# Kernel tuning notes

Measured on AMD Instinct MI355X. Metric: run time of the kernel, lower is better.

The kernel has to match this reference:

```python
import jax, jax.numpy as jnp
import numpy as np

N_HEAD = 16

def setup_inputs() -> dict:
    key = jax.random.key(0)
    k0, k1, k2, k3 = jax.random.split(key, 4)
    S, E, H, T = 2048, 1024, N_HEAD, 4096
    d = E // H
    return {
        "x": jax.random.normal(k0, (S, E), jnp.float32),
        "past": jax.random.normal(k1, (2, H, T, d), jnp.float32),  # stacked [pk, pv]
        "W1": jax.random.normal(k2, (E, 3 * E), jnp.float32) * 0.02,  # c_attn (Conv1D k=1 == linear)
        "b1": jnp.zeros((3 * E,), jnp.float32),
        "W2": jax.random.normal(k3, (E, E), jnp.float32) * 0.02,  # c_proj
        "b2": jnp.zeros((E,), jnp.float32),
        "past_length": 2048,
    }


def reference(x, past, W1, b1, W2, b2, past_length):
    H = N_HEAD
    S, E = x.shape
    d = E // H

    c = x @ W1 + b1  # [S, 3E]
    q, k, v = jnp.split(c, 3, axis=1)

    def split_heads(t):  # [S, E] -> [H, S, d]
        return jnp.transpose(t.reshape(S, H, d), (1, 0, 2))

    q, k, v = split_heads(q), split_heads(k), split_heads(v)

    pk, pv = past[0], past[1]  # [H, T, d]
    k = jax.lax.dynamic_update_slice_in_dim(pk, k, past_length, axis=1)
    v = jax.lax.dynamic_update_slice_in_dim(pv, v, past_length, axis=1)

    # attention scores [H, S, T]
    w = jnp.einsum('hid,hjd->hij', q, k) / np.sqrt(d)
    ns = k.shape[1]
    i = jnp.arange(S)[:, None]
    j = jnp.arange(ns)[None, :]
    b = (i >= j - past_length).astype(w.dtype)
    w = w * b - jnp.float32(1e10) * (1 - b)
    w = jax.nn.softmax(w, axis=-1)

    a = jnp.einsum('hij,hjd->hid', w, v)  # [H, S, d]
    # faithful to original: start index clamps to 0 since axis len == S
    a = jax.lax.dynamic_slice_in_dim(a, past_length, S, axis=1)
    a = jnp.transpose(a, (1, 0, 2)).reshape(S, E)  # merge heads

    out = a @ W2 + b2
    new_cache = jnp.stack([k, v], axis=0)
    return out, new_cache
```

## Files before the change

kernel.cpp:

```cpp
#include <hip/hip_runtime.h>
#include <hip/hip_bf16.h>
#include <stdint.h>


#define S_LEN 2048
#define E_DIM 1024
#define NHEAD 16
#define HDIM  64
#define T_LEN 4096
#define PASTL 2048

typedef __bf16 bf16x8 __attribute__((ext_vector_type(8)));
typedef __bf16 bf16x4 __attribute__((ext_vector_type(4)));
typedef __bf16 bf16x2 __attribute__((ext_vector_type(2)));
typedef float  f32x4  __attribute__((ext_vector_type(4)));
typedef float  f32x16 __attribute__((ext_vector_type(16)));
typedef unsigned u32x2 __attribute__((ext_vector_type(2)));

static __device__ __forceinline__ f32x4 mfma_bf16(bf16x8 a, bf16x8 b, f32x4 c) {
  return __builtin_amdgcn_mfma_f32_16x16x32_bf16(a, b, c, 0, 0, 0);
}
static __device__ __forceinline__ f32x16 mfma32(bf16x8 a, bf16x8 b, f32x16 c) {
  return __builtin_amdgcn_mfma_f32_32x32x16_bf16(a, b, c, 0, 0, 0);
}

static __device__ __forceinline__ unsigned int f2bf(float f) {
  union { float f; unsigned int u; } v; v.f = f;
  unsigned int u = v.u;
  return (u + 0x7fffu + ((u >> 16) & 1u)) >> 16;
}

static __device__ __forceinline__ float bf2f(unsigned short u) {
  union { unsigned int u; float f; } v; v.u = (unsigned int)u << 16;
  return v.f;
}

static __device__ __forceinline__ unsigned pkbf(float lo, float hi) {
  bf16x2 t = {(__bf16)lo, (__bf16)hi};
  return __builtin_bit_cast(unsigned, t);
}

#define GLOBAL_LOAD_LDS16(gptr, lptr)                                              \
  __builtin_amdgcn_global_load_lds(                                                \
      (const __attribute__((address_space(1))) unsigned int*)(gptr),               \
      (__attribute__((address_space(3))) unsigned int*)(lptr), 16, 0, 0)

__global__ __launch_bounds__(256) void prep_kernel(
    const float* __restrict__ past, const float* __restrict__ x,
    const float* __restrict__ W1, const float* __restrict__ W2,
    float* __restrict__ cache, unsigned short* __restrict__ kb,
    unsigned short* __restrict__ xb, unsigned short* __restrict__ w1t,
    unsigned short* __restrict__ w2t, unsigned short* __restrict__ vtb) {
  __shared__ float tile[64][65];
  const int bid = blockIdx.x;
  const int tid = threadIdx.x;
  const int tx = tid & 63, ty = tid >> 6;

  if (bid < 512) {
    const int h = bid >> 5;
    const int t0 = (bid & 31) * 64;
    const float* in = past + (size_t)(NHEAD + h) * T_LEN * HDIM;
    unsigned short* outp = vtb + (size_t)h * HDIM * T_LEN;
#pragma unroll
    for (int r = 0; r < 64; r += 4)
      tile[r + ty][tx] = in[(size_t)(t0 + r + ty) * HDIM + tx];
    __syncthreads();
#pragma unroll
    for (int r = 0; r < 64; r += 4)
      outp[(size_t)(r + ty) * T_LEN + t0 + tx] = f2bf(tile[tx][r + ty]);
  } else if (bid < 1536) {
    const float* in;
    unsigned short* outp;
    int rows, cols, c0, r0;
    if (bid < 1280) {
      int u = bid - 512;
      in = W1; outp = w1t; rows = 1024; cols = 3072;
      c0 = (u % 48) * 64; r0 = (u / 48) * 64;
    } else {
      int u = bid - 1280;
      in = W2; outp = w2t; rows = 1024; cols = 1024;
      c0 = (u & 15) * 64; r0 = (u >> 4) * 64;
    }
#pragma unroll
    for (int r = 0; r < 64; r += 4)
      tile[r + ty][tx] = in[(size_t)(r0 + r + ty) * cols + c0 + tx];
    __syncthreads();
#pragma unroll
    for (int r = 0; r < 64; r += 4)
      outp[(size_t)(c0 + r + ty) * rows + r0 + tx] = f2bf(tile[tx][r + ty]);
  } else {
    const int n4p = (2 * NHEAD * PASTL * HDIM) / 4;
    const int n4x = (S_LEN * E_DIM) / 4;
    for (int i = (bid - 1536) * 256 + tid; i < n4p + n4x; i += 2048 * 256) {
      if (i < n4p) {
        int e = i * 4;
        int d = e & 63;
        int t = (e >> 6) & (PASTL - 1);
        int hh = (e >> 17) & (NHEAD - 1);
        int kv = e >> 21;
        size_t full = (((size_t)kv * NHEAD + hh) * T_LEN + t) * HDIM + d;
        float4 v = *(const float4*)(past + full);
        *(float4*)(cache + full) = v;
        if (kv == 0) {
          ushort4 u;
          u.x = f2bf(v.x); u.y = f2bf(v.y); u.z = f2bf(v.z); u.w = f2bf(v.w);
          *(ushort4*)(kb + full) = u;
        }
      } else {
        int j = i - n4p;
        float4 v = ((const float4*)x)[j];
        ushort4 u;
        u.x = f2bf(v.x); u.y = f2bf(v.y); u.z = f2bf(v.z); u.w = f2bf(v.w);
        ((ushort4*)xb)[j] = u;
      }
    }
  }
}

template <int MODE>
__global__ __launch_bounds__(256) void gemm_bt_kernel(
    const unsigned short* __restrict__ A, const unsigned short* __restrict__ Bt,
    const float* __restrict__ bias, int K,
    float* __restrict__ out_f32, unsigned short* __restrict__ qb,
    float* __restrict__ cache_k, float* __restrict__ cache_v,
    unsigned short* __restrict__ kb, unsigned short* __restrict__ vtb) {
  __shared__ alignas(16) unsigned short As[2][64 * 64];
  __shared__ alignas(16) unsigned short Bs[2][128 * 64];
  const int NPX = (MODE == 0) ? 3 : 1;
  const int bid = blockIdx.x;
  const int xcd = bid & 7;
  const int loc = bid >> 3;
  const int n_idx = xcd * NPX + loc % NPX;
  const int m_idx = loc / NPX;
  const int m0 = m_idx * 64, n0 = n_idx * 128;

  const int tid = threadIdx.x;
  const int lane = tid & 63;
  const int w = tid >> 6;
  const int wm = w >> 1, wn = w & 1;
  const int lr = lane & 15;
  const int lg = lane >> 4;

  f32x4 acc[2][4];
#pragma unroll
  for (int i = 0; i < 2; ++i)
#pragma unroll
    for (int j = 0; j < 4; ++j) acc[i][j] = f32x4{0.f, 0.f, 0.f, 0.f};

  const int srow = tid >> 3;
  const int sseg = (tid & 7) ^ (srow & 7);
  const unsigned short* ga0 = A + (size_t)(m0 + srow) * K + sseg * 8;
  const unsigned short* gb0 = Bt + (size_t)(n0 + srow) * K + sseg * 8;

  auto stage = [&](int b, int k0) {
    GLOBAL_LOAD_LDS16(ga0 + k0, (char*)As[b] + tid * 16);
    GLOBAL_LOAD_LDS16(ga0 + (size_t)32 * K + k0, (char*)As[b] + 4096 + tid * 16);
#pragma unroll
    for (int j = 0; j < 4; ++j)
      GLOBAL_LOAD_LDS16(gb0 + (size_t)(32 * j) * K + k0,
                        (char*)Bs[b] + j * 4096 + tid * 16);
  };

  const int NKS = K >> 6;
  stage(0, 0);
  int cur = 0;
  for (int i = 0; i < NKS; ++i) {
    asm volatile("s_waitcnt vmcnt(0)" ::: "memory");
    __builtin_amdgcn_s_barrier();
    __builtin_amdgcn_sched_barrier(0);
    if (i + 1 < NKS) stage(cur ^ 1, (i + 1) * 64);

#pragma unroll
    for (int kk = 0; kk < 2; ++kk) {
      bf16x8 af[2], bfr[4];
#pragma unroll
      for (int mi = 0; mi < 2; ++mi) {
        int row = wm * 32 + mi * 16 + lr;
        int slot = (kk * 4 + lg) ^ (row & 7);
        af[mi] = *reinterpret_cast<const bf16x8*>((const char*)As[cur] + row * 128 + slot * 16);
      }
#pragma unroll
      for (int ni = 0; ni < 4; ++ni) {
        int row = wn * 64 + ni * 16 + lr;
        int slot = (kk * 4 + lg) ^ (row & 7);
        bfr[ni] = *reinterpret_cast<const bf16x8*>((const char*)Bs[cur] + row * 128 + slot * 16);
      }
#pragma unroll
      for (int mi = 0; mi < 2; ++mi)
#pragma unroll
        for (int ni = 0; ni < 4; ++ni)
          acc[mi][ni] = mfma_bf16(af[mi], bfr[ni], acc[mi][ni]);
    }
    cur ^= 1;
  }

#pragma unroll
  for (int ni = 0; ni < 4; ++ni) {
    int n = n0 + wn * 64 + ni * 16 + lr;
    float bv = bias[n];
#pragma unroll
    for (int mi = 0; mi < 2; ++mi) {
      int mbase = m0 + wm * 32 + mi * 16 + lg * 4;
      float v4[4];
#pragma unroll
      for (int r = 0; r < 4; ++r) v4[r] = acc[mi][ni][r] + bv;
      if (MODE == 0) {
        if (n < E_DIM) {
#pragma unroll
          for (int r = 0; r < 4; ++r)
            qb[(size_t)(mbase + r) * E_DIM + n] = f2bf(v4[r] * 0.18033688f);
        } else if (n < 2 * E_DIM) {
          int e = n - E_DIM;
          size_t base = ((size_t)(e >> 6) * T_LEN + (PASTL + mbase)) * HDIM + (e & 63);
#pragma unroll
          for (int r = 0; r < 4; ++r) {
            cache_k[base + (size_t)r * HDIM] = v4[r];
            kb[base + (size_t)r * HDIM] = f2bf(v4[r]);
          }
        } else {
          int e = n - 2 * E_DIM;
          int hh = e >> 6, d = e & 63;
          size_t base = ((size_t)hh * T_LEN + (PASTL + mbase)) * HDIM + d;
#pragma unroll
          for (int r = 0; r < 4; ++r) cache_v[base + (size_t)r * HDIM] = v4[r];
          ushort4 u;
          u.x = f2bf(v4[0]); u.y = f2bf(v4[1]);
          u.z = f2bf(v4[2]); u.w = f2bf(v4[3]);
          *(ushort4*)(vtb + ((size_t)hh * HDIM + d) * T_LEN + PASTL + mbase) = u;
        }
      } else {
#pragma unroll
        for (int r = 0; r < 4; ++r)
          out_f32[(size_t)(mbase + r) * E_DIM + n] = v4[r];
      }
    }
  }
}

__global__ __launch_bounds__(256) void attn_kernel(
    const unsigned short* __restrict__ qb, const unsigned short* __restrict__ kb,
    const unsigned short* __restrict__ vt,
    unsigned short* __restrict__ o_part, float* __restrict__ l_part) {
  __shared__ alignas(16) unsigned short Ks[2][64 * 64];
  __shared__ alignas(16) unsigned short Vs[2][64 * 64];
  const int fid = blockIdx.x;
  const int h = (fid & 7) + ((fid >= 448) ? 8 : 0);
  const int g = (fid >> 3) - ((fid >= 448) ? 56 : 0);
  int x, c;
  if (g < 24) { x = g / 3; c = g - 3 * x; }
  else { int g2 = g - 24; x = 8 + (g2 >> 2); c = g2 & 3; }

  const int tid = threadIdx.x;
  const int w = tid >> 6;
  const int lane = tid & 63;
  const int l31 = lane & 31;
  const int hi = lane >> 5;
  const int hi4 = hi * 4;
  const int q0 = x * 128 + w * 32;

  const unsigned short* qrow = qb + (size_t)(q0 + l31) * E_DIM + h * HDIM + hi * 8;
  bf16x8 qf[4];
#pragma unroll
  for (int kk = 0; kk < 4; ++kk)
    qf[kk] = *reinterpret_cast<const bf16x8*>(qrow + kk * 16);

  const unsigned short* kh = kb + (size_t)h * T_LEN * HDIM;
  const unsigned short* vh = vt + (size_t)h * HDIM * T_LEN;

  const int srow = tid >> 3;
  const int sseg = (tid & 7) ^ (srow & 7);
  const unsigned short* ksrc = kh + (size_t)srow * HDIM + sseg * 8;
  const unsigned short* vsrc = vh + (size_t)srow * T_LEN + sseg * 8;

  f32x16 o0, o1, zc;
#pragma unroll
  for (int i = 0; i < 16; ++i) { o0[i] = 0.f; o1[i] = 0.f; zc[i] = 0.f; }
  float lsum = 0.f;

  const int NTfull = 34 + 2 * x;
  const int tb = c * 16;
  const int te = (tb + 16 < NTfull) ? tb + 16 : NTfull;
  const int NT = te - tb;
  const int tbeg = tb * 64;
  const int qpp = q0 + l31 + PASTL;

  auto stageK = [&](int b, int t0) {
    GLOBAL_LOAD_LDS16(ksrc + (size_t)t0 * HDIM, (char*)Ks[b] + tid * 16);
    GLOBAL_LOAD_LDS16(ksrc + (size_t)(t0 + 32) * HDIM, (char*)Ks[b] + 4096 + tid * 16);
  };
  auto stageV = [&](int b, int t0) {
    GLOBAL_LOAD_LDS16(vsrc + t0, (char*)Vs[b] + tid * 16);
    GLOBAL_LOAD_LDS16(vsrc + t0 + (size_t)32 * T_LEN, (char*)Vs[b] + 4096 + tid * 16);
  };

  stageK(0, tbeg);
  stageV(0, tbeg);
  int cur = 0;
  int t0 = tbeg;
  for (int i = 0; i < NT; ++i, t0 += 64) {
    const bool more = (i + 1 < NT);
    asm volatile("s_waitcnt vmcnt(2)" ::: "memory");
    __builtin_amdgcn_s_barrier();
    __builtin_amdgcn_sched_barrier(0);
    if (more) stageK(cur ^ 1, t0 + 64);

    f32x16 s0, s1;
    __builtin_amdgcn_s_setprio(1);
    {
      int sl = hi ^ (l31 & 7);
      bf16x8 k0 = *reinterpret_cast<const bf16x8*>((const char*)Ks[cur] + l31 * 128 + sl * 16);
      bf16x8 k1 = *reinterpret_cast<const bf16x8*>((const char*)Ks[cur] + (32 + l31) * 128 + sl * 16);
      s0 = mfma32(k0, qf[0], zc);
      s1 = mfma32(k1, qf[0], zc);
    }
#pragma unroll
    for (int kk = 1; kk < 4; ++kk) {
      int sl = (kk * 2 + hi) ^ (l31 & 7);
      bf16x8 k0 = *reinterpret_cast<const bf16x8*>((const char*)Ks[cur] + l31 * 128 + sl * 16);
      bf16x8 k1 = *reinterpret_cast<const bf16x8*>((const char*)Ks[cur] + (32 + l31) * 128 + sl * 16);
      s0 = mfma32(k0, qf[kk], s0);
      s1 = mfma32(k1, qf[kk], s1);
    }
    __builtin_amdgcn_s_setprio(0);

    const bool partial = (t0 + 63 > q0 + PASTL);
    unsigned aw[8], bw[8];
    if (!partial) {
#pragma unroll
      for (int i2 = 0; i2 < 8; ++i2) {
        float p0 = __builtin_amdgcn_exp2f(s0[2 * i2]);
        float p1 = __builtin_amdgcn_exp2f(s0[2 * i2 + 1]);
        float p2 = __builtin_amdgcn_exp2f(s1[2 * i2]);
        float p3 = __builtin_amdgcn_exp2f(s1[2 * i2 + 1]);
        lsum += (p0 + p1) + (p2 + p3);
        aw[i2] = pkbf(p0, p1);
        bw[i2] = pkbf(p2, p3);
      }
    } else {
      const int thr = qpp - t0;
#pragma unroll
      for (int i2 = 0; i2 < 8; ++i2) {
        int r0 = 2 * i2;
        int ko = (r0 & 3) + 8 * (r0 >> 2) + hi4;
        float p0 = __builtin_amdgcn_exp2f(s0[r0]);
        float p1 = __builtin_amdgcn_exp2f(s0[r0 + 1]);
        float p2 = __builtin_amdgcn_exp2f(s1[r0]);
        float p3 = __builtin_amdgcn_exp2f(s1[r0 + 1]);
        if (ko > thr) p0 = 0.f;
        if (ko + 1 > thr) p1 = 0.f;
        if (ko + 32 > thr) p2 = 0.f;
        if (ko + 33 > thr) p3 = 0.f;
        lsum += (p0 + p1) + (p2 + p3);
        aw[i2] = pkbf(p0, p1);
        bw[i2] = pkbf(p2, p3);
      }
    }

    union U4 { unsigned u[4]; bf16x8 v; };
    U4 pa0, pa1, pa2, pa3;
    {
      u32x2 r02 = __builtin_amdgcn_permlane32_swap(aw[0], aw[2], false, false);
      u32x2 r13 = __builtin_amdgcn_permlane32_swap(aw[1], aw[3], false, false);
      pa0.u[0] = r02[0]; pa0.u[1] = r13[0]; pa0.u[2] = r02[1]; pa0.u[3] = r13[1];
      u32x2 r46 = __builtin_amdgcn_permlane32_swap(aw[4], aw[6], false, false);
      u32x2 r57 = __builtin_amdgcn_permlane32_swap(aw[5], aw[7], false, false);
      pa1.u[0] = r46[0]; pa1.u[1] = r57[0]; pa1.u[2] = r46[1]; pa1.u[3] = r57[1];
      u32x2 s02 = __builtin_amdgcn_permlane32_swap(bw[0], bw[2], false, false);
      u32x2 s13 = __builtin_amdgcn_permlane32_swap(bw[1], bw[3], false, false);
      pa2.u[0] = s02[0]; pa2.u[1] = s13[0]; pa2.u[2] = s02[1]; pa2.u[3] = s13[1];
      u32x2 s46 = __builtin_amdgcn_permlane32_swap(bw[4], bw[6], false, false);
      u32x2 s57 = __builtin_amdgcn_permlane32_swap(bw[5], bw[7], false, false);
      pa3.u[0] = s46[0]; pa3.u[1] = s57[0]; pa3.u[2] = s46[1]; pa3.u[3] = s57[1];
    }

    if (more) {
      asm volatile("s_waitcnt vmcnt(2)" ::: "memory");
    } else {
      asm volatile("s_waitcnt vmcnt(0)" ::: "memory");
    }
    __builtin_amdgcn_s_barrier();
    __builtin_amdgcn_sched_barrier(0);
    if (more) stageV(cur ^ 1, t0 + 64);

    __builtin_amdgcn_s_setprio(1);
    {
      int sl = hi ^ (l31 & 7);
      bf16x8 v0 = *reinterpret_cast<const bf16x8*>((const char*)Vs[cur] + l31 * 128 + sl * 16);
      bf16x8 v1 = *reinterpret_cast<const bf16x8*>((const char*)Vs[cur] + (32 + l31) * 128 + sl * 16);
      o0 = mfma32(pa0.v, v0, o0);
      o1 = mfma32(pa0.v, v1, o1);
    }
    {
      int sl = (2 + hi) ^ (l31 & 7);
      bf16x8 v0 = *reinterpret_cast<const bf16x8*>((const char*)Vs[cur] + l31 * 128 + sl * 16);
      bf16x8 v1 = *reinterpret_cast<const bf16x8*>((const char*)Vs[cur] + (32 + l31) * 128 + sl * 16);
      o0 = mfma32(pa1.v, v0, o0);
      o1 = mfma32(pa1.v, v1, o1);
    }
    {
      int sl = (4 + hi) ^ (l31 & 7);
      bf16x8 v0 = *reinterpret_cast<const bf16x8*>((const char*)Vs[cur] + l31 * 128 + sl * 16);
      bf16x8 v1 = *reinterpret_cast<const bf16x8*>((const char*)Vs[cur] + (32 + l31) * 128 + sl * 16);
      o0 = mfma32(pa2.v, v0, o0);
      o1 = mfma32(pa2.v, v1, o1);
    }
    {
      int sl = (6 + hi) ^ (l31 & 7);
      bf16x8 v0 = *reinterpret_cast<const bf16x8*>((const char*)Vs[cur] + l31 * 128 + sl * 16);
      bf16x8 v1 = *reinterpret_cast<const bf16x8*>((const char*)Vs[cur] + (32 + l31) * 128 + sl * 16);
      o0 = mfma32(pa3.v, v0, o0);
      o1 = mfma32(pa3.v, v1, o1);
    }
    __builtin_amdgcn_s_setprio(0);
    cur ^= 1;
  }

  lsum += __shfl_xor(lsum, 32);

  unsigned short* op = o_part + ((size_t)(c * NHEAD + h) * S_LEN) * HDIM;
  float* lp = l_part + (size_t)(c * NHEAD + h) * S_LEN;
  if (hi == 0) lp[q0 + l31] = lsum;
#pragma unroll
  for (int r = 0; r < 16; ++r) {
    int qr = (r & 3) + 8 * (r >> 2) + hi4;
    op[(size_t)(q0 + qr) * HDIM + l31] = f2bf(o0[r]);
    op[(size_t)(q0 + qr) * HDIM + 32 + l31] = f2bf(o1[r]);
  }
}

__global__ __launch_bounds__(256) void attn_merge_kernel(
    const unsigned short* __restrict__ o_part, const float* __restrict__ l_part,
    unsigned short* __restrict__ ab) {
  const int flat = blockIdx.x * 256 + threadIdx.x;
  const int d4 = flat & 15;
  const int row = (flat >> 4) & (S_LEN - 1);
  const int h = flat >> 15;
  const int nc = (row < 1024) ? 3 : 4;
  const size_t cstride_o = (size_t)NHEAD * S_LEN * HDIM;
  const size_t base_o = (((size_t)h * S_LEN) + row) * HDIM + d4 * 4;
  float acc[4] = {0.f, 0.f, 0.f, 0.f};
  float l = 0.f;
  for (int cc = 0; cc < nc; ++cc) {
    ushort4 u = *(const ushort4*)(o_part + cc * cstride_o + base_o);
    acc[0] += bf2f(u.x); acc[1] += bf2f(u.y);
    acc[2] += bf2f(u.z); acc[3] += bf2f(u.w);
    l += l_part[(size_t)cc * NHEAD * S_LEN + (size_t)h * S_LEN + row];
  }
  float inv = 1.f / l;
  ushort4 u;
  u.x = f2bf(acc[0] * inv);
  u.y = f2bf(acc[1] * inv);
  u.z = f2bf(acc[2] * inv);
  u.w = f2bf(acc[3] * inv);
  *(ushort4*)(ab + (size_t)row * E_DIM + h * HDIM + d4 * 4) = u;
}


extern "C" void kernel_launch(void* const* d_in, const int* in_sizes, int n_in,
                              void* d_out, int out_size, void* d_ws, size_t ws_size,
                              hipStream_t stream) {
  (void)in_sizes; (void)n_in; (void)out_size; (void)ws_size;
  const float* x    = (const float*)d_in[0];
  const float* past = (const float*)d_in[1];
  const float* W1   = (const float*)d_in[2];
  const float* b1   = (const float*)d_in[3];
  const float* W2   = (const float*)d_in[4];
  const float* b2   = (const float*)d_in[5];

  float* out = (float*)d_out;
  float* cache_k = out + (size_t)S_LEN * E_DIM;
  float* cache_v = cache_k + (size_t)NHEAD * T_LEN * HDIM;

  char* ws = (char*)d_ws;
  unsigned short* w2t = (unsigned short*)(ws);
  unsigned short* qb  = (unsigned short*)(ws + (size_t)(2u  << 20));
  unsigned short* kb  = (unsigned short*)(ws + (size_t)(6u  << 20));
  unsigned short* vtb = (unsigned short*)(ws + (size_t)(14u << 20));
  unsigned short* xb  = (unsigned short*)(ws + (size_t)(22u << 20));
  unsigned short* ab  = (unsigned short*)(ws + (size_t)(22u << 20));
  unsigned short* w1t = (unsigned short*)(ws + (size_t)(26u << 20));
  unsigned short* o_part = (unsigned short*)(ws + (size_t)(26u << 20));
  float* l_part = (float*)(ws + (size_t)(42u << 20));

  prep_kernel<<<3584, 256, 0, stream>>>(past, x, W1, W2, cache_k, kb, xb, w1t,
                                        w2t, vtb);
  gemm_bt_kernel<0><<<768, 256, 0, stream>>>(
      xb, w1t, b1, 1024, nullptr, qb, cache_k, cache_v, kb, vtb);
  attn_kernel<<<dim3(896), 256, 0, stream>>>(qb, kb, vtb, o_part, l_part);
  attn_merge_kernel<<<(NHEAD * S_LEN * 16) / 256, 256, 0, stream>>>(o_part, l_part, ab);
  gemm_bt_kernel<1><<<256, 256, 0, stream>>>(
      ab, w2t, b2, 1024, out, nullptr, nullptr, nullptr, nullptr, nullptr);
}
```

Baseline: 118.9 us.

## Widen attention KV tile from 64 to 128 keys per iteration

Each loop iteration of the attention kernel now stages and processes 128 keys instead of 64, with larger double-buffered K and V shared-memory tiles and a new V swizzle layout for 256-byte rows. The aim is to halve the number of barriers and pipeline steps per chunk and give more MFMA work between synchronisations. The cost is doubled LDS use, which can cut occupancy, and more registers for the eight P fragments held across the loop. Masking is adjusted with a per-half offset.

```diff
diff --git a/kernel.cpp b/kernel.cpp
--- a/kernel.cpp
+++ b/kernel.cpp
@@ -241,8 +241,8 @@
     const unsigned short* __restrict__ qb, const unsigned short* __restrict__ kb,
     const unsigned short* __restrict__ vt,
     unsigned short* __restrict__ o_part, float* __restrict__ l_part) {
-  __shared__ alignas(16) unsigned short Ks[2][64 * 64];
-  __shared__ alignas(16) unsigned short Vs[2][64 * 64];
+  __shared__ alignas(16) unsigned short Ks[2][128 * 64];
+  __shared__ alignas(16) unsigned short Vs[2][64 * 128];
   const int fid = blockIdx.x;
   const int h = (fid & 7) + ((fid >= 448) ? 8 : 0);
   const int g = (fid >> 3) - ((fid >= 448) ? 56 : 0);
@@ -270,146 +270,145 @@
   const int srow = tid >> 3;
   const int sseg = (tid & 7) ^ (srow & 7);
   const unsigned short* ksrc = kh + (size_t)srow * HDIM + sseg * 8;
-  const unsigned short* vsrc = vh + (size_t)srow * T_LEN + sseg * 8;
+  const int vrow = tid >> 4;
+  const int vseg = (tid & 15) ^ (vrow & 7);
+  const unsigned short* vsrc = vh + (size_t)vrow * T_LEN + vseg * 8;
 
   f32x16 o0, o1, zc;
 #pragma unroll
   for (int i = 0; i < 16; ++i) { o0[i] = 0.f; o1[i] = 0.f; zc[i] = 0.f; }
   float lsum = 0.f;
 
-  const int NTfull = 34 + 2 * x;
-  const int tb = c * 16;
-  const int te = (tb + 16 < NTfull) ? tb + 16 : NTfull;
+  const int NT2full = 17 + x;
+  const int tb = c * 8;
+  const int te = (tb + 8 < NT2full) ? tb + 8 : NT2full;
   const int NT = te - tb;
-  const int tbeg = tb * 64;
+  const int tbeg = tb * 128;
   const int qpp = q0 + l31 + PASTL;
 
   auto stageK = [&](int b, int t0) {
-    GLOBAL_LOAD_LDS16(ksrc + (size_t)t0 * HDIM, (char*)Ks[b] + tid * 16);
-    GLOBAL_LOAD_LDS16(ksrc + (size_t)(t0 + 32) * HDIM, (char*)Ks[b] + 4096 + tid * 16);
+#pragma unroll
+    for (int j = 0; j < 4; ++j)
+      GLOBAL_LOAD_LDS16(ksrc + (size_t)(t0 + 32 * j) * HDIM,
+                        (char*)Ks[b] + j * 4096 + tid * 16);
   };
   auto stageV = [&](int b, int t0) {
-    GLOBAL_LOAD_LDS16(vsrc + t0, (char*)Vs[b] + tid * 16);
-    GLOBAL_LOAD_LDS16(vsrc + t0 + (size_t)32 * T_LEN, (char*)Vs[b] + 4096 + tid * 16);
+#pragma unroll
+    for (int j = 0; j < 4; ++j)
+      GLOBAL_LOAD_LDS16(vsrc + (size_t)(16 * j) * T_LEN + t0,
+                        (char*)Vs[b] + j * 4096 + tid * 16);
   };
 
   stageK(0, tbeg);
   stageV(0, tbeg);
   int cur = 0;
   int t0 = tbeg;
-  for (int i = 0; i < NT; ++i, t0 += 64) {
+  for (int i = 0; i < NT; ++i, t0 += 128) {
     const bool more = (i + 1 < NT);
-    asm volatile("s_waitcnt vmcnt(2)" ::: "memory");
+    asm volatile("s_waitcnt vmcnt(4)" ::: "memory");
     __builtin_amdgcn_s_barrier();
     __builtin_amdgcn_sched_barrier(0);
-    if (more) stageK(cur ^ 1, t0 + 64);
-
-    f32x16 s0, s1;
-    __builtin_amdgcn_s_setprio(1);
-    {
-      int sl = hi ^ (l31 & 7);
-      bf16x8 k0 = *reinterpret_cast<const bf16x8*>((const char*)Ks[cur] + l31 * 128 + sl * 16);
-      bf16x8 k1 = *reinterpret_cast<const bf16x8*>((const char*)Ks[cur] + (32 + l31) * 128 + sl * 16);
-      s0 = mfma32(k0, qf[0], zc);
-      s1 = mfma32(k1, qf[0], zc);
-    }
-#pragma unroll
-    for (int kk = 1; kk < 4; ++kk) {
-      int sl = (kk * 2 + hi) ^ (l31 & 7);
-      bf16x8 k0 = *reinterpret_cast<const bf16x8*>((const char*)Ks[cur] + l31 * 128 + sl * 16);
-      bf16x8 k1 = *reinterpret_cast<const bf16x8*>((const char*)Ks[cur] + (32 + l31) * 128 + sl * 16);
-      s0 = mfma32(k0, qf[kk], s0);
-      s1 = mfma32(k1, qf[kk], s1);
-    }
-    __builtin_amdgcn_s_setprio(0);
-
-    const bool partial = (t0 + 63 > q0 + PASTL);
-    unsigned aw[8], bw[8];
-    if (!partial) {
-#pragma unroll
-      for (int i2 = 0; i2 < 8; ++i2) {
-        float p0 = __builtin_amdgcn_exp2f(s0[2 * i2]);
-        float p1 = __builtin_amdgcn_exp2f(s0[2 * i2 + 1]);
-        float p2 = __builtin_amdgcn_exp2f(s1[2 * i2]);
-        float p3 = __builtin_amdgcn_exp2f(s1[2 * i2 + 1]);
-        lsum += (p0 + p1) + (p2 + p3);
-        aw[i2] = pkbf(p0, p1);
-        bw[i2] = pkbf(p2, p3);
-      }
-    } else {
-      const int thr = qpp - t0;
-#pragma unroll
-      for (int i2 = 0; i2 < 8; ++i2) {
-        int r0 = 2 * i2;
-        int ko = (r0 & 3) + 8 * (r0 >> 2) + hi4;
-        float p0 = __builtin_amdgcn_exp2f(s0[r0]);
-        float p1 = __builtin_amdgcn_exp2f(s0[r0 + 1]);
-        float p2 = __builtin_amdgcn_exp2f(s1[r0]);
-        float p3 = __builtin_amdgcn_exp2f(s1[r0 + 1]);
-        if (ko > thr) p0 = 0.f;
-        if (ko + 1 > thr) p1 = 0.f;
-        if (ko + 32 > thr) p2 = 0.f;
-        if (ko + 33 > thr) p3 = 0.f;
-        lsum += (p0 + p1) + (p2 + p3);
-        aw[i2] = pkbf(p0, p1);
-        bw[i2] = pkbf(p2, p3);
-      }
-    }
-
+    if (more) stageK(cur ^ 1, t0 + 128);
+
+    const bool partial = (t0 + 127 > q0 + PASTL);
+    const int thr = qpp - t0;
     union U4 { unsigned u[4]; bf16x8 v; };
-    U4 pa0, pa1, pa2, pa3;
-    {
-      u32x2 r02 = __builtin_amdgcn_permlane32_swap(aw[0], aw[2], false, false);
-      u32x2 r13 = __builtin_amdgcn_permlane32_swap(aw[1], aw[3], false, false);
-      pa0.u[0] = r02[0]; pa0.u[1] = r13[0]; pa0.u[2] = r02[1]; pa0.u[3] = r13[1];
-      u32x2 r46 = __builtin_amdgcn_permlane32_swap(aw[4], aw[6], false, false);
-      u32x2 r57 = __builtin_amdgcn_permlane32_swap(aw[5], aw[7], false, false);
-      pa1.u[0] = r46[0]; pa1.u[1] = r57[0]; pa1.u[2] = r46[1]; pa1.u[3] = r57[1];
-      u32x2 s02 = __builtin_amdgcn_permlane32_swap(bw[0], bw[2], false, false);
-      u32x2 s13 = __builtin_amdgcn_permlane32_swap(bw[1], bw[3], false, false);
-      pa2.u[0] = s02[0]; pa2.u[1] = s13[0]; pa2.u[2] = s02[1]; pa2.u[3] = s13[1];
-      u32x2 s46 = __builtin_amdgcn_permlane32_swap(bw[4], bw[6], false, false);
-      u32x2 s57 = __builtin_amdgcn_permlane32_swap(bw[5], bw[7], false, false);
-      pa3.u[0] = s46[0]; pa3.u[1] = s57[0]; pa3.u[2] = s46[1]; pa3.u[3] = s57[1];
+    U4 pa[8];
+#pragma unroll
+    for (int half = 0; half < 2; ++half) {
+      const int rbA = half * 2, rbB = half * 2 + 1;
+      f32x16 sA, sB;
+      __builtin_amdgcn_s_setprio(1);
+      {
+        int rA = rbA * 32 + l31, rB = rbB * 32 + l31;
+        int slA = hi ^ (rA & 7), slB = hi ^ (rB & 7);
+        bf16x8 kA = *reinterpret_cast<const bf16x8*>((const char*)Ks[cur] + rA * 128 + slA * 16);
+        bf16x8 kB = *reinterpret_cast<const bf16x8*>((const char*)Ks[cur] + rB * 128 + slB * 16);
+        sA = mfma32(kA, qf[0], zc);
+        sB = mfma32(kB, qf[0], zc);
+      }
+#pragma unroll
+      for (int kk = 1; kk < 4; ++kk) {
+        int rA = rbA * 32 + l31, rB = rbB * 32 + l31;
+        int slA = (kk * 2 + hi) ^ (rA & 7), slB = (kk * 2 + hi) ^ (rB & 7);
+        bf16x8 kA = *reinterpret_cast<const bf16x8*>((const char*)Ks[cur] + rA * 128 + slA * 16);
+        bf16x8 kB = *reinterpret_cast<const bf16x8*>((const char*)Ks[cur] + rB * 128 + slB * 16);
+        sA = mfma32(kA, qf[kk], sA);
+        sB = mfma32(kB, qf[kk], sB);
+      }
+      __builtin_amdgcn_s_setprio(0);
+
+      unsigned aw[8], bw[8];
+      if (!partial) {
+#pragma unroll
+        for (int i2 = 0; i2 < 8; ++i2) {
+          float p0 = __builtin_amdgcn_exp2f(sA[2 * i2]);
+          float p1 = __builtin_amdgcn_exp2f(sA[2 * i2 + 1]);
+          float p2 = __builtin_amdgcn_exp2f(sB[2 * i2]);
+          float p3 = __builtin_amdgcn_exp2f(sB[2 * i2 + 1]);
+          lsum += (p0 + p1) + (p2 + p3);
+          aw[i2] = pkbf(p0, p1);
+          bw[i2] = pkbf(p2, p3);
+        }
+      } else {
+        const int bo = half * 64;
+#pragma unroll
+        for (int i2 = 0; i2 < 8; ++i2) {
+          int r0 = 2 * i2;
+          int ko = (r0 & 3) + 8 * (r0 >> 2) + hi4 + bo;
+          float p0 = __builtin_amdgcn_exp2f(sA[r0]);
+          float p1 = __builtin_amdgcn_exp2f(sA[r0 + 1]);
+          float p2 = __builtin_amdgcn_exp2f(sB[r0]);
+          float p3 = __builtin_amdgcn_exp2f(sB[r0 + 1]);
+          if (ko > thr) p0 = 0.f;
+          if (ko + 1 > thr) p1 = 0.f;
+          if (ko + 32 > thr) p2 = 0.f;
+          if (ko + 33 > thr) p3 = 0.f;
+          lsum += (p0 + p1) + (p2 + p3);
+          aw[i2] = pkbf(p0, p1);
+          bw[i2] = pkbf(p2, p3);
+        }
+      }
+
+      {
+        u32x2 r02 = __builtin_amdgcn_permlane32_swap(aw[0], aw[2], false, false);
+        u32x2 r13 = __builtin_amdgcn_permlane32_swap(aw[1], aw[3], false, false);
+        pa[4 * half + 0].u[0] = r02[0]; pa[4 * half + 0].u[1] = r13[0];
+        pa[4 * half + 0].u[2] = r02[1]; pa[4 * half + 0].u[3] = r13[1];
+        u32x2 r46 = __builtin_amdgcn_permlane32_swap(aw[4], aw[6], false, false);
+        u32x2 r57 = __builtin_amdgcn_permlane32_swap(aw[5], aw[7], false, false);
+        pa[4 * half + 1].u[0] = r46[0]; pa[4 * half + 1].u[1] = r57[0];
+        pa[4 * half + 1].u[2] = r46[1]; pa[4 * half + 1].u[3] = r57[1];
+        u32x2 s02 = __builtin_amdgcn_permlane32_swap(bw[0], bw[2], false, false);
+        u32x2 s13 = __builtin_amdgcn_permlane32_swap(bw[1], bw[3], false, false);
+        pa[4 * half + 2].u[0] = s02[0]; pa[4 * half + 2].u[1] = s13[0];
+        pa[4 * half + 2].u[2] = s02[1]; pa[4 * half + 2].u[3] = s13[1];
+        u32x2 s46 = __builtin_amdgcn_permlane32_swap(bw[4], bw[6], false, false);
+        u32x2 s57 = __builtin_amdgcn_permlane32_swap(bw[5], bw[7], false, false);
+        pa[4 * half + 3].u[0] = s46[0]; pa[4 * half + 3].u[1] = s57[0];
+        pa[4 * half + 3].u[2] = s46[1]; pa[4 * half + 3].u[3] = s57[1];
+      }
     }
 
     if (more) {
-      asm volatile("s_waitcnt vmcnt(2)" ::: "memory");
+      asm volatile("s_waitcnt vmcnt(4)" ::: "memory");
     } else {
       asm volatile("s_waitcnt vmcnt(0)" ::: "memory");
     }
     __builtin_amdgcn_s_barrier();
     __builtin_amdgcn_sched_barrier(0);
-    if (more) stageV(cur ^ 1, t0 + 64);
+    if (more) stageV(cur ^ 1, t0 + 128);
 
     __builtin_amdgcn_s_setprio(1);
-    {
-      int sl = hi ^ (l31 & 7);
-      bf16x8 v0 = *reinterpret_cast<const bf16x8*>((const char*)Vs[cur] + l31 * 128 + sl * 16);
-      bf16x8 v1 = *reinterpret_cast<const bf16x8*>((const char*)Vs[cur] + (32 + l31) * 128 + sl * 16);
-      o0 = mfma32(pa0.v, v0, o0);
-      o1 = mfma32(pa0.v, v1, o1);
-    }
-    {
-      int sl = (2 + hi) ^ (l31 & 7);
-      bf16x8 v0 = *reinterpret_cast<const bf16x8*>((const char*)Vs[cur] + l31 * 128 + sl * 16);
-      bf16x8 v1 = *reinterpret_cast<const bf16x8*>((const char*)Vs[cur] + (32 + l31) * 128 + sl * 16);
-      o0 = mfma32(pa1.v, v0, o0);
-      o1 = mfma32(pa1.v, v1, o1);
-    }
-    {
-      int sl = (4 + hi) ^ (l31 & 7);
-      bf16x8 v0 = *reinterpret_cast<const bf16x8*>((const char*)Vs[cur] + l31 * 128 + sl * 16);
-      bf16x8 v1 = *reinterpret_cast<const bf16x8*>((const char*)Vs[cur] + (32 + l31) * 128 + sl * 16);
-      o0 = mfma32(pa2.v, v0, o0);
-      o1 = mfma32(pa2.v, v1, o1);
-    }
-    {
-      int sl = (6 + hi) ^ (l31 & 7);
-      bf16x8 v0 = *reinterpret_cast<const bf16x8*>((const char*)Vs[cur] + l31 * 128 + sl * 16);
-      bf16x8 v1 = *reinterpret_cast<const bf16x8*>((const char*)Vs[cur] + (32 + l31) * 128 + sl * 16);
-      o0 = mfma32(pa3.v, v0, o0);
-      o1 = mfma32(pa3.v, v1, o1);
+#pragma unroll
+    for (int ks = 0; ks < 8; ++ks) {
+      int d0 = l31, d1 = 32 + l31;
+      int sl0 = (2 * ks + hi) ^ (d0 & 7);
+      int sl1 = (2 * ks + hi) ^ (d1 & 7);
+      bf16x8 v0 = *reinterpret_cast<const bf16x8*>((const char*)Vs[cur] + d0 * 256 + sl0 * 16);
+      bf16x8 v1 = *reinterpret_cast<const bf16x8*>((const char*)Vs[cur] + d1 * 256 + sl1 * 16);
+      o0 = mfma32(pa[ks].v, v0, o0);
+      o1 = mfma32(pa[ks].v, v1, o1);
     }
     __builtin_amdgcn_s_setprio(0);
     cur ^= 1;
```

New measurement: 111.9 us. -5.9%, faster.
